# Optimization experiments

Hardware: AMD Instinct MI355X
Metric: run time of the kernel (lower is better)

Reference implementation:

```python
import math
import jax, jax.numpy as jnp
import numpy as np

STEP = 0.1
EPS = 1e-12


def _laplacian(src, dst, n):
    # dense symmetric-normalized Laplacian from COO edge list (symmetrized, 0/1 weights)
    A = jnp.zeros((n, n), dtype=jnp.float32).at[src, dst].set(1.0)
    A = jnp.maximum(A, A.T)
    deg = A.sum(axis=1)
    dinv = jnp.where(deg > 0, 1.0 / jnp.sqrt(jnp.maximum(deg, 1e-12)), 0.0)
    return jnp.eye(n, dtype=jnp.float32) - dinv[:, None] * A * dinv[None, :]


def _filter_bank(L, bs):
    # rational band-pass bank centered at b in arange(0,2.1,STEP):
    # D_b = sqrt(2)*a * inv((L - b I)^4 + a I),  a = (STEP/2)^4
    n = L.shape[0]
    a = (STEP / 2.0) ** 4
    I = jnp.eye(n, dtype=L.dtype)

    def one(b):
        M1 = L - b * I
        P2 = M1 @ M1
        P4 = P2 @ P2
        return math.sqrt(2.0) * a * jnp.linalg.inv(P4 + a * I)

    return jax.vmap(one)(bs)  # [F, n, n]


def _cdist_mean(e):
    # mean pairwise euclidean distance, safe sqrt on the zero diagonal
    d2 = jnp.sum((e[:, None, :] - e[None, :, :]) ** 2, axis=-1)
    d = jnp.sqrt(jnp.where(d2 > 0, d2, 1.0))
    return jnp.where(d2 > 0, d, 0.0).mean()


def setup_inputs() -> dict:
    key = jax.random.key(0)
    k1, k2, k3, k4, k5 = jax.random.split(key, 5)
    B, N, F0, R, E = 64, 128, 32, 1118, 512
    return {
        "x": jax.random.normal(k1, (B, N, F0), dtype=jnp.float32),
        "random_signal": jax.random.normal(k2, (B, N, R), dtype=jnp.float32),
        "C": jax.random.normal(k3, (21, 1), dtype=jnp.float32),
        "edge_src": jax.random.randint(k4, (B, E), 0, N),
        "edge_dst": jax.random.randint(k5, (B, E), 0, N),
        "num_classes": 4,
    }


def reference(x, random_signal, C, edge_src, edge_dst, num_classes):
    B, N, _ = x.shape
    R = random_signal.shape[-1]
    # torch.normal(0, sqrt(1/R)) random signal concatenated to features
    feats = jnp.concatenate([x, random_signal * math.sqrt(1.0 / R)], axis=-1)  # [B,N,F0+R]
    bs = jnp.arange(0.0, 2.1, STEP, dtype=jnp.float32)  # [21]
    Cn = C / jnp.maximum(jnp.linalg.norm(C, axis=0, keepdims=True), EPS)  # F.normalize(C, dim=0)

    def per_graph(src, dst, xg):
        L = _laplacian(src, dst, N)
        D = _filter_bank(L, bs)                      # [F,N,N]
        L_hat = jnp.einsum('fnm,f->nm', D, Cn[:, 0])  # D.permute(1,2,0) @ C, squeezed
        A_hat = jnp.eye(N, dtype=xg.dtype) - L_hat
        y = A_hat @ xg                                # [N, F0+R]
        z = y / jnp.maximum(jnp.linalg.norm(y, axis=1, keepdims=True), EPS)
        logits = z @ z.T                              # decode_all on normalized x
        sp = -jnp.abs(logits).sum() / (N * N)         # -||logits||_1 / n^2
        return y.mean(axis=0), sp

    emb, sp_terms = jax.vmap(per_graph)(edge_src, edge_dst, feats)  # [B,D], [B]

    # faithful repeated in-loop division: s_{i+1} = (s_i + t_i)/B  =>  sum_i t_i * B^{-(B-i)}
    i = jnp.arange(B, dtype=jnp.float32)
    w = jnp.exp(-(B - i) * jnp.log(float(B)))
    sparsity_fwd = jnp.sum(sp_terms * w)

    # labels y = arange(B) % num_classes; one positive group (class members) and
    # one negative group (non-members) per class
    idx = np.arange(B)
    hl1 = jnp.float32(0.0)
    hl2 = jnp.float32(0.0)
    for c in range(num_classes):
        pos = jnp.asarray(idx[idx % num_classes == c])
        neg = jnp.asarray(idx[idx % num_classes != c])
        beta = 1.0 / num_classes + 1e-13  # one group per class
        hl1 = hl1 + (-_cdist_mean(emb[neg])) / beta
        hl2 = hl2 + _cdist_mean(emb[pos])

    Fk = C.shape[0]
    dims = jnp.sqrt(jnp.float32(Fk))
    c_l1 = jnp.sum(jnp.abs(C), axis=0)
    c_l2 = jnp.maximum(jnp.linalg.norm(C, axis=0), EPS)
    sparsity_c = jnp.mean((dims - c_l1 / c_l2) / (dims - 1.0))

    return sparsity_c + hl2 + hl1 + sparsity_fwd
```

## Files before the change

### kernel.cpp

```cpp
#include <hip/hip_runtime.h>
#include <math.h>

#define NN 128
#define SM 129
#define TS 132
#define RS 132
#define SS 17
#define SD 130
#define EP 132

typedef double d4 __attribute__((ext_vector_type(4)));

__global__ __launch_bounds__(256) void k1_lap(
    const int* __restrict__ src, const int* __restrict__ dst,
    int E, float* __restrict__ Lout) {
  extern __shared__ float sm1[];
  float* A    = sm1;
  float* dinv = sm1 + NN * SM;
  const int g   = blockIdx.x;
  const int tid = threadIdx.x;

  for (int e = tid; e < NN * NN; e += 256) {
    int i = e >> 7, j = e & 127;
    A[i * SM + j] = 0.f;
  }
  __syncthreads();
  const int* s = src + (size_t)g * E;
  const int* d = dst + (size_t)g * E;
  for (int e = tid; e < E; e += 256) {
    int a = s[e], b = d[e];
    A[a * SM + b] = 1.f;
    A[b * SM + a] = 1.f;
  }
  __syncthreads();
  if (tid < NN) {
    float acc = 0.f;
    for (int j = 0; j < NN; ++j) acc += A[tid * SM + j];
    dinv[tid] = (acc > 0.f) ? (float)(1.0 / sqrt((double)acc)) : 0.f;
  }
  __syncthreads();
  float* Lg = Lout + (size_t)g * NN * NN;
  for (int e = tid; e < NN * NN; e += 256) {
    int i = e >> 7, j = e & 127;
    Lg[e] = ((i == j) ? 1.f : 0.f) - dinv[i] * dinv[j] * A[i * SM + j];
  }
}

__global__ __launch_bounds__(512, 1) void kpow2(
    const float* __restrict__ L, double* __restrict__ L2) {
  extern __shared__ double Bs[];
  const int bid = blockIdx.x;
  const int g = bid >> 2, q = bid & 3;
  const int tid = threadIdx.x;
  const int wv = tid >> 6, ln = tid & 63;
  const int m  = ln & 15, kq = ln >> 4;
  const int rb = 32 * q + 16 * (wv & 1);
  const int cb0 = 2 * (wv >> 1);

  int rIdx[4], cIdx[4];
  {
    d4 z = {0.0, 0.0, 0.0, 0.0};
    d4 pr = __builtin_amdgcn_mfma_f64_16x16x4f64((double)m, 1.0, z, 0, 0, 0);
    d4 pc = __builtin_amdgcn_mfma_f64_16x16x4f64(1.0, (double)m, z, 0, 0, 0);
#pragma unroll
    for (int r = 0; r < 4; ++r) {
      rIdx[r] = ((int)(pr[r] * 0.25 + 0.5)) & 15;
      cIdx[r] = ((int)(pc[r] * 0.25 + 0.5)) & 15;
    }
  }

  const float* Lg = L + (size_t)g * NN * NN;
  for (int e = tid; e < NN * NN; e += 512) {
    int i = e >> 7, j = e & 127;
    Bs[i * SD + j] = (double)Lg[e];
  }
  __syncthreads();

  d4 acc[2];
#pragma unroll
  for (int c = 0; c < 2; ++c) {
    acc[c][0] = 0.0; acc[c][1] = 0.0; acc[c][2] = 0.0; acc[c][3] = 0.0;
  }
  for (int kc = 0; kc < 32; ++kc) {
    double a = Bs[(rb + m) * SD + 4 * kc + kq];
#pragma unroll
    for (int c = 0; c < 2; ++c) {
      double b = Bs[(4 * kc + kq) * SD + 16 * (cb0 + c) + m];
      acc[c] = __builtin_amdgcn_mfma_f64_16x16x4f64(a, b, acc[c], 0, 0, 0);
    }
  }
  double* out = L2 + (size_t)g * NN * NN;
#pragma unroll
  for (int c = 0; c < 2; ++c)
#pragma unroll
    for (int r = 0; r < 4; ++r)
      out[(rb + rIdx[r]) * NN + 16 * (cb0 + c) + cIdx[r]] = acc[c][r];
}

__global__ __launch_bounds__(512, 1) void kpow34(
    const float* __restrict__ L, const double* __restrict__ L2,
    double* __restrict__ L3, double* __restrict__ L4) {
  extern __shared__ double Bs[];
  const int bid = blockIdx.x;
  const int g = bid >> 2, h = (bid >> 1) & 1, job = bid & 1;
  const int tid = threadIdx.x;
  const int wv = tid >> 6, ln = tid & 63;
  const int m  = ln & 15, kq = ln >> 4;
  const int rb = 64 * h + 16 * (wv & 3);
  const int cb0 = 4 * (wv >> 2);

  int rIdx[4], cIdx[4];
  {
    d4 z = {0.0, 0.0, 0.0, 0.0};
    d4 pr = __builtin_amdgcn_mfma_f64_16x16x4f64((double)m, 1.0, z, 0, 0, 0);
    d4 pc = __builtin_amdgcn_mfma_f64_16x16x4f64(1.0, (double)m, z, 0, 0, 0);
#pragma unroll
    for (int r = 0; r < 4; ++r) {
      rIdx[r] = ((int)(pr[r] * 0.25 + 0.5)) & 15;
      cIdx[r] = ((int)(pc[r] * 0.25 + 0.5)) & 15;
    }
  }

  const float*  Lg  = L  + (size_t)g * NN * NN;
  const double* L2g = L2 + (size_t)g * NN * NN;
  if (job == 0) {
    for (int e = tid; e < NN * NN; e += 512) {
      int i = e >> 7, j = e & 127;
      Bs[i * SD + j] = (double)Lg[e];
    }
  } else {
    for (int e = tid; e < NN * NN; e += 512) {
      int i = e >> 7, j = e & 127;
      Bs[i * SD + j] = L2g[e];
    }
  }
  __syncthreads();

  d4 acc[4];
#pragma unroll
  for (int c = 0; c < 4; ++c) {
    acc[c][0] = 0.0; acc[c][1] = 0.0; acc[c][2] = 0.0; acc[c][3] = 0.0;
  }
  for (int kc = 0; kc < 32; ++kc) {
    double a = L2g[(rb + m) * NN + 4 * kc + kq];
#pragma unroll
    for (int c = 0; c < 4; ++c) {
      double b = Bs[(4 * kc + kq) * SD + 16 * (cb0 + c) + m];
      acc[c] = __builtin_amdgcn_mfma_f64_16x16x4f64(a, b, acc[c], 0, 0, 0);
    }
  }
  double* out = (job == 0 ? L3 : L4) + (size_t)g * NN * NN;
#pragma unroll
  for (int c = 0; c < 4; ++c)
#pragma unroll
    for (int r = 0; r < 4; ++r)
      out[(rb + rIdx[r]) * NN + 16 * (cb0 + c) + cIdx[r]] = acc[c][r];
}

__global__ __launch_bounds__(512, 4) void k2_filter(
    const float* __restrict__ L, const double* __restrict__ L2,
    const double* __restrict__ L3, const double* __restrict__ L4,
    const float* __restrict__ C, int NF, float* __restrict__ W) {
  extern __shared__ char smraw[];
  double* Rp  = (double*)smraw;
  double* Scd = (double*)(smraw + 16 * RS * 8);
  double* Pv  = (double*)(smraw + 16 * RS * 8 + 8 * 16 * SS * 8);

  const int bid = blockIdx.x;
  const int g = bid / NF, f = bid % NF;
  const int tid = threadIdx.x;
  const int wv = tid >> 6, ln = tid & 63;
  const int m  = ln & 15, kq = ln >> 4;
  double* S = Scd + wv * 16 * SS;

  double csum = 0.0;
  for (int q = 0; q < NF; ++q) { double c = (double)C[q]; csum += c * c; }
  double cn = sqrt(csum); if (cn < 1e-12) cn = 1e-12;
  const double a4 = 6.25e-6;
  const double coef = 1.4142135623730951 * a4 * ((double)C[f] / cn);
  const float  bf = (float)((double)f * 0.1);
  const double bb = (double)bf;
  const double c3 = -4.0 * bb;
  const double c2 = 6.0 * bb * bb;
  const double c1 = -4.0 * bb * bb * bb;
  const double c0 = bb * bb * bb * bb + a4;

  int rIdx[4], cIdx[4];
  {
    d4 z = {0.0, 0.0, 0.0, 0.0};
    d4 pr = __builtin_amdgcn_mfma_f64_16x16x4f64((double)m, 1.0, z, 0, 0, 0);
    d4 pc = __builtin_amdgcn_mfma_f64_16x16x4f64(1.0, (double)m, z, 0, 0, 0);
#pragma unroll
    for (int r = 0; r < 4; ++r) {
      rIdx[r] = ((int)(pr[r] * 0.25 + 0.5)) & 15;
      cIdx[r] = ((int)(pc[r] * 0.25 + 0.5)) & 15;
    }
  }

  const float*  Lg  = L  + (size_t)g * NN * NN;
  const double* L2g = L2 + (size_t)g * NN * NN;
  const double* L3g = L3 + (size_t)g * NN * NN;
  const double* L4g = L4 + (size_t)g * NN * NN;
  d4 T[8];
#pragma unroll
  for (int cb = 0; cb < 8; ++cb)
#pragma unroll
    for (int r = 0; r < 4; ++r) {
      int i = 16 * wv + rIdx[r], j = 16 * cb + cIdx[r];
      int idx = i * NN + j;
      double v = L4g[idx];
      v = fma(c3, L3g[idx], v);
      v = fma(c2, L2g[idx], v);
      v = fma(c1, (double)Lg[idx], v);
      if (i == j) v += c0;
      T[cb][r] = v;
    }

#pragma unroll 1
  for (int t = 0; t < 8; ++t) {
    if (wv == t) {
#pragma unroll
      for (int cb = 0; cb < 8; ++cb)
#pragma unroll
        for (int r = 0; r < 4; ++r)
          Rp[rIdx[r] * RS + 16 * cb + cIdx[r]] = T[cb][r];
    }
    __syncthreads();

    if (wv == t) {
      double sr[4];
#pragma unroll
      for (int r = 0; r < 4; ++r) sr[r] = Rp[(4 * r + kq) * RS + 16 * t + m];
#pragma unroll
      for (int k = 0; k < 16; ++k) {
        const int kr = k >> 2, kl = k & 3;
        double pv   = __shfl(sr[kr], 16 * kl + k);
        double rowv = __shfl(sr[kr], 16 * kl + m);
        double cv[4];
#pragma unroll
        for (int r = 0; r < 4; ++r) cv[r] = __shfl(sr[r], 16 * kq + k);
        double dp = 1.0 / pv;
#pragma unroll
        for (int r = 0; r < 4; ++r) {
          int i = 4 * r + kq;
          double nv;
          if (i == k)      nv = (m == k) ? dp : rowv * dp;
          else if (m == k) nv = -cv[r] * dp;
          else             nv = fma(-(cv[r] * dp), rowv, sr[r]);
          sr[r] = nv;
        }
      }
#pragma unroll
      for (int r = 0; r < 4; ++r) Pv[(4 * r + kq) * SS + m] = sr[r];
    }
    __syncthreads();

#pragma unroll
    for (int cb = 0; cb < 8; ++cb) {
      if (cb != t) continue;
      if (wv == t) {
#pragma unroll
        for (int r = 0; r < 4; ++r) T[cb][r] = Pv[rIdx[r] * SS + cIdx[r]];
      } else {
#pragma unroll
        for (int r = 0; r < 4; ++r) S[rIdx[r] * SS + cIdx[r]] = T[cb][r];
        __builtin_amdgcn_wave_barrier();
        d4 ncv = {0.0, 0.0, 0.0, 0.0};
#pragma unroll
        for (int kc = 0; kc < 4; ++kc) {
          double a = S[m * SS + 4 * kc + kq];
          double b = -Pv[(4 * kc + kq) * SS + m];
          ncv = __builtin_amdgcn_mfma_f64_16x16x4f64(a, b, ncv, 0, 0, 0);
        }
        T[cb] = ncv;
        __builtin_amdgcn_wave_barrier();
#pragma unroll
        for (int r = 0; r < 4; ++r) S[rIdx[r] * SS + cIdx[r]] = T[cb][r];
      }
    }
    __builtin_amdgcn_wave_barrier();

    const double* asrc = (wv == t) ? Pv : S;
#pragma unroll
    for (int cb = 0; cb < 8; ++cb) {
      if (cb == t) continue;
      d4 acc;
      if (wv == t) { acc[0] = 0.0; acc[1] = 0.0; acc[2] = 0.0; acc[3] = 0.0; }
      else         { acc = T[cb]; }
#pragma unroll
      for (int kc = 0; kc < 4; ++kc) {
        double a = asrc[m * SS + 4 * kc + kq];
        double b = Rp[(4 * kc + kq) * RS + 16 * cb + m];
        acc = __builtin_amdgcn_mfma_f64_16x16x4f64(a, b, acc, 0, 0, 0);
      }
      T[cb] = acc;
    }
    __syncthreads();
  }

  float* Wg = W + (size_t)g * NN * NN;
#pragma unroll
  for (int cb = 0; cb < 8; ++cb)
#pragma unroll
    for (int r = 0; r < 4; ++r)
      atomicAdd(&Wg[(16 * wv + rIdx[r]) * NN + 16 * cb + cIdx[r]],
                (float)(coef * T[cb][r]));
}

__global__ __launch_bounds__(512, 4) void k3_fused(
    const float* __restrict__ x, const float* __restrict__ rs,
    const float* __restrict__ W, float* __restrict__ G,
    float* __restrict__ emb, int F0, int R, int DTOT, int NCH,
    float rscale) {
  extern __shared__ float sm3[];
  float* ldsX = sm3;
  float* embA = sm3 + NN * TS;
  const int bid = blockIdx.x;
  const int g = bid / NCH;
  const int c = bid % NCH;
  const int d0 = c * 128;
  const int tid = threadIdx.x, tr = tid >> 4, tc = tid & 15;

  const float* xg = x + (size_t)g * NN * F0;
  const float* rg = rs + (size_t)g * NN * R;
  for (int e = tid; e < NN * NN; e += 512) {
    int k = e >> 7, dl = e & 127;
    int d = d0 + dl;
    float v = 0.f;
    if (d < DTOT) v = (d < F0) ? xg[k * F0 + d] : rg[k * R + (d - F0)] * rscale;
    ldsX[k * TS + dl] = v;
  }
  if (tid < NN) embA[tid] = 0.f;
  __syncthreads();

  const float* Wg = W + (size_t)g * NN * NN;
  float acc[4][8];
#pragma unroll
  for (int v = 0; v < 4; ++v)
#pragma unroll
    for (int u = 0; u < 8; ++u) acc[v][u] = 0.f;
  float4 w4 = *(const float4*)(Wg + 4 * tr);
  for (int k = 0; k < NN; ++k) {
    float4 w4n;
    if (k < NN - 1) w4n = *(const float4*)(Wg + (k + 1) * NN + 4 * tr);
    float xv[8];
#pragma unroll
    for (int u = 0; u < 8; ++u) xv[u] = ldsX[k * TS + tc + 16 * u];
    float wvv[4] = {w4.x, w4.y, w4.z, w4.w};
#pragma unroll
    for (int v = 0; v < 4; ++v)
#pragma unroll
      for (int u = 0; u < 8; ++u) acc[v][u] = fmaf(wvv[v], xv[u], acc[v][u]);
    w4 = w4n;
  }
#pragma unroll
  for (int v = 0; v < 4; ++v)
#pragma unroll
    for (int u = 0; u < 8; ++u)
      acc[v][u] = ldsX[(4 * tr + v) * TS + tc + 16 * u] - acc[v][u];

#pragma unroll
  for (int u = 0; u < 8; ++u) {
    float s = acc[0][u] + acc[1][u] + acc[2][u] + acc[3][u];
    atomicAdd(&embA[tc + 16 * u], s);
  }
  __syncthreads();

#pragma unroll
  for (int v = 0; v < 4; ++v)
#pragma unroll
    for (int u = 0; u < 8; ++u)
      ldsX[(tc + 16 * u) * TS + 4 * tr + v] = acc[v][u];
  __syncthreads();

  if (tid < 128) {
    int d = d0 + tid;
    if (d < DTOT) emb[(size_t)g * 1152 + d] = embA[tid] * (1.f / 128.f);
  }

  float gg[4][8];
#pragma unroll
  for (int v = 0; v < 4; ++v)
#pragma unroll
    for (int u = 0; u < 8; ++u) gg[v][u] = 0.f;
  for (int dl = 0; dl < NN; ++dl) {
    float4 a4v = *(const float4*)(ldsX + dl * TS + 4 * tr);
    float bv[8];
#pragma unroll
    for (int u = 0; u < 8; ++u) bv[u] = ldsX[dl * TS + tc + 16 * u];
    float av[4] = {a4v.x, a4v.y, a4v.z, a4v.w};
#pragma unroll
    for (int v = 0; v < 4; ++v)
#pragma unroll
      for (int u = 0; u < 8; ++u) gg[v][u] = fmaf(av[v], bv[u], gg[v][u]);
  }
  float* Gg = G + (size_t)g * NN * NN;
#pragma unroll
  for (int v = 0; v < 4; ++v)
#pragma unroll
    for (int u = 0; u < 8; ++u)
      atomicAdd(&Gg[(4 * tr + v) * NN + tc + 16 * u], gg[v][u]);
}

__global__ __launch_bounds__(256) void k45_fused(
    const float* __restrict__ G, double* __restrict__ spt,
    const float* __restrict__ emb, float* __restrict__ Dm, int DTOT) {
  __shared__ float inr[NN];
  __shared__ double red[4];
  const int bid = blockIdx.x, tid = threadIdx.x;
  if (bid < 64) {
    const int g = bid;
    const float* Gg = G + (size_t)g * NN * NN;
    if (tid < NN) {
      float n = sqrtf(fmaxf(Gg[tid * NN + tid], 0.f));
      inr[tid] = 1.f / fmaxf(n, 1e-12f);
    }
    __syncthreads();
    double s = 0.0;
    for (int e = tid; e < NN * NN; e += 256) {
      int i = e >> 7, j = e & 127;
      s += (double)(fabsf(Gg[e]) * inr[i] * inr[j]);
    }
    for (int off = 32; off; off >>= 1) s += __shfl_down(s, off);
    int wave = tid >> 6, lane = tid & 63;
    if (lane == 0) red[wave] = s;
    __syncthreads();
    if (tid == 0) spt[g] = -(red[0] + red[1] + red[2] + red[3]) / (double)(NN * NN);
  } else {
    const int i = bid - 64;
    const int wv = tid >> 6, l = tid & 63;
    float ei[18];
#pragma unroll
    for (int s = 0; s < 18; ++s) {
      int d = l + 64 * s;
      ei[s] = (d < DTOT) ? emb[(size_t)i * 1152 + d] : 0.f;
    }
    for (int jj = 0; jj < 16; ++jj) {
      int j = 4 * jj + wv;
      float acc = 0.f;
#pragma unroll
      for (int s = 0; s < 18; ++s) {
        int d = l + 64 * s;
        if (d < DTOT) {
          float df = ei[s] - emb[(size_t)j * 1152 + d];
          acc = fmaf(df, df, acc);
        }
      }
      for (int off = 32; off; off >>= 1) acc += __shfl_down(acc, off);
      if (l == 0) Dm[i * 64 + j] = (acc > 0.f) ? sqrtf(acc) : 0.f;
    }
  }
}

__global__ __launch_bounds__(64) void k5b_final(
    const float* __restrict__ Dm, const double* __restrict__ spt,
    const float* __restrict__ C, int NF,
    const int* __restrict__ ncls, float* __restrict__ out) {
  const int lane = threadIdx.x;
  const int nc = ncls[0];
  double spf = spt[lane] * exp(-((double)(64 - lane)) * log(64.0));
  for (int off = 32; off; off >>= 1) spf += __shfl_down(spf, off);

  double hl1 = 0.0, hl2 = 0.0;
  const double beta = 1.0 / (double)nc + 1e-13;
  for (int cc = 0; cc < nc; ++cc) {
    bool ip = (lane % nc) == cc;
    double ps = 0.0, ns = 0.0;
    for (int j = 0; j < 64; ++j) {
      double dv = (double)Dm[lane * 64 + j];
      bool jp = (j % nc) == cc;
      if (ip && jp) ps += dv;
      if (!ip && !jp) ns += dv;
    }
    for (int off = 32; off; off >>= 1) {
      ps += __shfl_down(ps, off);
      ns += __shfl_down(ns, off);
    }
    int npos = 0;
    for (int q = 0; q < 64; ++q) if (q % nc == cc) npos++;
    int nneg = 64 - npos;
    hl2 += ps / ((double)npos * (double)npos);
    hl1 += -(ns / ((double)nneg * (double)nneg)) / beta;
  }
  if (lane == 0) {
    double l1 = 0.0, l2 = 0.0;
    for (int q = 0; q < NF; ++q) { double cv = (double)C[q]; l1 += fabs(cv); l2 += cv * cv; }
    l2 = sqrt(l2); if (l2 < 1e-12) l2 = 1e-12;
    double dims = sqrt((double)NF);
    double sc = (dims - l1 / l2) / (dims - 1.0);
    out[0] = (float)(sc + hl2 + hl1 + spf);
  }
}

extern "C" void kernel_launch(void* const* d_in, const int* in_sizes, int n_in,
                              void* d_out, int out_size, void* d_ws, size_t ws_size,
                              hipStream_t stream) {
  (void)n_in; (void)out_size; (void)ws_size;
  const float* x    = (const float*)d_in[0];
  const float* rs   = (const float*)d_in[1];
  const float* C    = (const float*)d_in[2];
  const int*   esrc = (const int*)d_in[3];
  const int*   edst = (const int*)d_in[4];
  const int*   ncls = (const int*)d_in[5];
  float* out = (float*)d_out;

  const int F0   = in_sizes[0] / (64 * 128);
  const int R    = in_sizes[1] / (64 * 128);
  const int NF   = in_sizes[2];
  const int E    = in_sizes[3] / 64;
  const int DTOT = F0 + R;
  const int NCH  = (DTOT + 127) / 128;
  const float rscale = (float)(1.0 / sqrt((double)R));

  char* ws = (char*)d_ws;
  size_t off = 0;
  float*  L    = (float*)(ws + off);  off += (size_t)64 * NN * NN * 4;
  float*  W    = (float*)(ws + off);  off += (size_t)64 * NN * NN * 4;
  float*  G    = (float*)(ws + off);  off += (size_t)64 * NN * NN * 4;
  double* L2d  = (double*)(ws + off); off += (size_t)64 * NN * NN * 8;
  double* L3d  = (double*)(ws + off); off += (size_t)64 * NN * NN * 8;
  double* L4d  = (double*)(ws + off); off += (size_t)64 * NN * NN * 8;
  float*  emb  = (float*)(ws + off);  off += (size_t)64 * 1152 * 4;
  double* spt  = (double*)(ws + off); off += (size_t)64 * 8;
  float*  Dm   = (float*)(ws + off);  off += (size_t)64 * 64 * 4;

  hipMemsetAsync(W, 0, (size_t)2 * 64 * NN * NN * 4, stream);

  const int lds1 = (NN * SM + NN) * 4;
  const int ldsp = NN * SD * 8;
  const int lds2 = 16 * RS * 8 + 8 * 16 * SS * 8 + 16 * SS * 8;
  const int lds3 = (NN * TS + NN) * 4;
  hipFuncSetAttribute((const void*)k1_lap,    hipFuncAttributeMaxDynamicSharedMemorySize, lds1);
  hipFuncSetAttribute((const void*)kpow2,     hipFuncAttributeMaxDynamicSharedMemorySize, ldsp);
  hipFuncSetAttribute((const void*)kpow34,    hipFuncAttributeMaxDynamicSharedMemorySize, ldsp);
  hipFuncSetAttribute((const void*)k2_filter, hipFuncAttributeMaxDynamicSharedMemorySize, lds2);
  hipFuncSetAttribute((const void*)k3_fused,  hipFuncAttributeMaxDynamicSharedMemorySize, lds3);

  k1_lap<<<64, 256, lds1, stream>>>(esrc, edst, E, L);
  kpow2<<<256, 512, ldsp, stream>>>(L, L2d);
  kpow34<<<256, 512, ldsp, stream>>>(L, L2d, L3d, L4d);
  k2_filter<<<64 * NF, 512, lds2, stream>>>(L, L2d, L3d, L4d, C, NF, W);
  k3_fused<<<64 * NCH, 512, lds3, stream>>>(x, rs, W, G, emb, F0, R, DTOT, NCH, rscale);
  k45_fused<<<128, 256, 0, stream>>>(G, spt, emb, Dm, DTOT);
  k5b_final<<<1, 64, 0, stream>>>(Dm, spt, C, NF, ncls, out);
}
```

Measured before the change: 601.8 us.

## Stage L as float in LDS and split matrix-power kernels into more blocks

The L², L³ and L⁴ kernels now keep L in LDS as fp32 instead of fp64, which halves the shared-memory footprint. Each block also computes fewer output tiles, so twice as many blocks launch with launch bounds that allow 4 blocks per CU. The L4 job now reads both operands of L2 straight from global memory and does not stage them in LDS, trading LDS traffic for cached global loads. The goal is better occupancy and latency hiding in these small fp64 MFMA GEMMs, but per-block staging overhead grows because each block reloads the whole matrix.

New measurement: 606.9 us. Within noise of the previous version (+0.9%).

```diff
diff --git a/kernel.cpp b/kernel.cpp
--- a/kernel.cpp
+++ b/kernel.cpp
@@ -6,7 +6,7 @@
 #define TS 132
 #define RS 132
 #define SS 17
-#define SD 130
+#define SF 132
 #define EP 132
 
 typedef double d4 __attribute__((ext_vector_type(4)));
@@ -46,11 +46,54 @@
   }
 }
 
-__global__ __launch_bounds__(512, 1) void kpow2(
+__global__ __launch_bounds__(512, 4) void kpow2(
     const float* __restrict__ L, double* __restrict__ L2) {
-  extern __shared__ double Bs[];
+  extern __shared__ float Bs[];
   const int bid = blockIdx.x;
-  const int g = bid >> 2, q = bid & 3;
+  const int g = bid >> 3, q = bid & 7;
+  const int tid = threadIdx.x;
+  const int wv = tid >> 6, ln = tid & 63;
+  const int m  = ln & 15, kq = ln >> 4;
+  const int rb = 16 * q;
+  const int cb = wv;
+
+  int rIdx[4], cIdx[4];
+  {
+    d4 z = {0.0, 0.0, 0.0, 0.0};
+    d4 pr = __builtin_amdgcn_mfma_f64_16x16x4f64((double)m, 1.0, z, 0, 0, 0);
+    d4 pc = __builtin_amdgcn_mfma_f64_16x16x4f64(1.0, (double)m, z, 0, 0, 0);
+#pragma unroll
+    for (int r = 0; r < 4; ++r) {
+      rIdx[r] = ((int)(pr[r] * 0.25 + 0.5)) & 15;
+      cIdx[r] = ((int)(pc[r] * 0.25 + 0.5)) & 15;
+    }
+  }
+
+  const float* Lg = L + (size_t)g * NN * NN;
+  for (int e4 = tid; e4 < (NN * NN) / 4; e4 += 512) {
+    int i = e4 >> 5, j4 = (e4 & 31) * 4;
+    *(float4*)(Bs + i * SF + j4) = *(const float4*)(Lg + i * NN + j4);
+  }
+  __syncthreads();
+
+  d4 acc = {0.0, 0.0, 0.0, 0.0};
+  for (int kc = 0; kc < 32; ++kc) {
+    double a = (double)Bs[(rb + m) * SF + 4 * kc + kq];
+    double b = (double)Bs[(4 * kc + kq) * SF + 16 * cb + m];
+    acc = __builtin_amdgcn_mfma_f64_16x16x4f64(a, b, acc, 0, 0, 0);
+  }
+  double* out = L2 + (size_t)g * NN * NN;
+#pragma unroll
+  for (int r = 0; r < 4; ++r)
+    out[(rb + rIdx[r]) * NN + 16 * cb + cIdx[r]] = acc[r];
+}
+
+__global__ __launch_bounds__(512, 4) void kpow34(
+    const float* __restrict__ L, const double* __restrict__ L2,
+    double* __restrict__ L3, double* __restrict__ L4) {
+  extern __shared__ float Bs[];
+  const int bid = blockIdx.x;
+  const int g = bid >> 3, q = (bid >> 1) & 3, job = bid & 1;
   const int tid = threadIdx.x;
   const int wv = tid >> 6, ln = tid & 63;
   const int m  = ln & 15, kq = ln >> 4;
@@ -69,89 +112,43 @@
     }
   }
 
-  const float* Lg = L + (size_t)g * NN * NN;
-  for (int e = tid; e < NN * NN; e += 512) {
-    int i = e >> 7, j = e & 127;
-    Bs[i * SD + j] = (double)Lg[e];
-  }
-  __syncthreads();
-
-  d4 acc[2];
-#pragma unroll
-  for (int c = 0; c < 2; ++c) {
-    acc[c][0] = 0.0; acc[c][1] = 0.0; acc[c][2] = 0.0; acc[c][3] = 0.0;
-  }
-  for (int kc = 0; kc < 32; ++kc) {
-    double a = Bs[(rb + m) * SD + 4 * kc + kq];
-#pragma unroll
-    for (int c = 0; c < 2; ++c) {
-      double b = Bs[(4 * kc + kq) * SD + 16 * (cb0 + c) + m];
-      acc[c] = __builtin_amdgcn_mfma_f64_16x16x4f64(a, b, acc[c], 0, 0, 0);
-    }
-  }
-  double* out = L2 + (size_t)g * NN * NN;
-#pragma unroll
-  for (int c = 0; c < 2; ++c)
-#pragma unroll
-    for (int r = 0; r < 4; ++r)
-      out[(rb + rIdx[r]) * NN + 16 * (cb0 + c) + cIdx[r]] = acc[c][r];
-}
-
-__global__ __launch_bounds__(512, 1) void kpow34(
-    const float* __restrict__ L, const double* __restrict__ L2,
-    double* __restrict__ L3, double* __restrict__ L4) {
-  extern __shared__ double Bs[];
-  const int bid = blockIdx.x;
-  const int g = bid >> 2, h = (bid >> 1) & 1, job = bid & 1;
-  const int tid = threadIdx.x;
-  const int wv = tid >> 6, ln = tid & 63;
-  const int m  = ln & 15, kq = ln >> 4;
-  const int rb = 64 * h + 16 * (wv & 3);
-  const int cb0 = 4 * (wv >> 2);
-
-  int rIdx[4], cIdx[4];
-  {
-    d4 z = {0.0, 0.0, 0.0, 0.0};
-    d4 pr = __builtin_amdgcn_mfma_f64_16x16x4f64((double)m, 1.0, z, 0, 0, 0);
-    d4 pc = __builtin_amdgcn_mfma_f64_16x16x4f64(1.0, (double)m, z, 0, 0, 0);
-#pragma unroll
-    for (int r = 0; r < 4; ++r) {
-      rIdx[r] = ((int)(pr[r] * 0.25 + 0.5)) & 15;
-      cIdx[r] = ((int)(pc[r] * 0.25 + 0.5)) & 15;
-    }
-  }
-
   const float*  Lg  = L  + (size_t)g * NN * NN;
   const double* L2g = L2 + (size_t)g * NN * NN;
   if (job == 0) {
-    for (int e = tid; e < NN * NN; e += 512) {
-      int i = e >> 7, j = e & 127;
-      Bs[i * SD + j] = (double)Lg[e];
+    for (int e4 = tid; e4 < (NN * NN) / 4; e4 += 512) {
+      int i = e4 >> 5, j4 = (e4 & 31) * 4;
+      *(float4*)(Bs + i * SF + j4) = *(const float4*)(Lg + i * NN + j4);
+    }
+  }
+  __syncthreads();
+
+  d4 acc[2];
+#pragma unroll
+  for (int c = 0; c < 2; ++c) {
+    acc[c][0] = 0.0; acc[c][1] = 0.0; acc[c][2] = 0.0; acc[c][3] = 0.0;
+  }
+  if (job == 0) {
+    for (int kc = 0; kc < 32; ++kc) {
+      double a = L2g[(rb + m) * NN + 4 * kc + kq];
+#pragma unroll
+      for (int c = 0; c < 2; ++c) {
+        double b = (double)Bs[(4 * kc + kq) * SF + 16 * (cb0 + c) + m];
+        acc[c] = __builtin_amdgcn_mfma_f64_16x16x4f64(a, b, acc[c], 0, 0, 0);
+      }
     }
   } else {
-    for (int e = tid; e < NN * NN; e += 512) {
-      int i = e >> 7, j = e & 127;
-      Bs[i * SD + j] = L2g[e];
-    }
-  }
-  __syncthreads();
-
-  d4 acc[4];
-#pragma unroll
-  for (int c = 0; c < 4; ++c) {
-    acc[c][0] = 0.0; acc[c][1] = 0.0; acc[c][2] = 0.0; acc[c][3] = 0.0;
-  }
-  for (int kc = 0; kc < 32; ++kc) {
-    double a = L2g[(rb + m) * NN + 4 * kc + kq];
-#pragma unroll
-    for (int c = 0; c < 4; ++c) {
-      double b = Bs[(4 * kc + kq) * SD + 16 * (cb0 + c) + m];
-      acc[c] = __builtin_amdgcn_mfma_f64_16x16x4f64(a, b, acc[c], 0, 0, 0);
+    for (int kc = 0; kc < 32; ++kc) {
+      double a = L2g[(rb + m) * NN + 4 * kc + kq];
+#pragma unroll
+      for (int c = 0; c < 2; ++c) {
+        double b = L2g[(4 * kc + kq) * NN + 16 * (cb0 + c) + m];
+        acc[c] = __builtin_amdgcn_mfma_f64_16x16x4f64(a, b, acc[c], 0, 0, 0);
+      }
     }
   }
   double* out = (job == 0 ? L3 : L4) + (size_t)g * NN * NN;
 #pragma unroll
-  for (int c = 0; c < 4; ++c)
+  for (int c = 0; c < 2; ++c)
 #pragma unroll
     for (int r = 0; r < 4; ++r)
       out[(rb + rIdx[r]) * NN + 16 * (cb0 + c) + cIdx[r]] = acc[c][r];
@@ -527,18 +524,18 @@
   hipMemsetAsync(W, 0, (size_t)2 * 64 * NN * NN * 4, stream);
 
   const int lds1 = (NN * SM + NN) * 4;
-  const int ldsp = NN * SD * 8;
+  const int ldsf = NN * SF * 4;
   const int lds2 = 16 * RS * 8 + 8 * 16 * SS * 8 + 16 * SS * 8;
   const int lds3 = (NN * TS + NN) * 4;
   hipFuncSetAttribute((const void*)k1_lap,    hipFuncAttributeMaxDynamicSharedMemorySize, lds1);
-  hipFuncSetAttribute((const void*)kpow2,     hipFuncAttributeMaxDynamicSharedMemorySize, ldsp);
-  hipFuncSetAttribute((const void*)kpow34,    hipFuncAttributeMaxDynamicSharedMemorySize, ldsp);
+  hipFuncSetAttribute((const void*)kpow2,     hipFuncAttributeMaxDynamicSharedMemorySize, ldsf);
+  hipFuncSetAttribute((const void*)kpow34,    hipFuncAttributeMaxDynamicSharedMemorySize, ldsf);
   hipFuncSetAttribute((const void*)k2_filter, hipFuncAttributeMaxDynamicSharedMemorySize, lds2);
   hipFuncSetAttribute((const void*)k3_fused,  hipFuncAttributeMaxDynamicSharedMemorySize, lds3);
 
   k1_lap<<<64, 256, lds1, stream>>>(esrc, edst, E, L);
-  kpow2<<<256, 512, ldsp, stream>>>(L, L2d);
-  kpow34<<<256, 512, ldsp, stream>>>(L, L2d, L3d, L4d);
+  kpow2<<<512, 512, ldsf, stream>>>(L, L2d);
+  kpow34<<<512, 512, ldsf, stream>>>(L, L2d, L3d, L4d);
   k2_filter<<<64 * NF, 512, lds2, stream>>>(L, L2d, L3d, L4d, C, NF, W);
   k3_fused<<<64 * NCH, 512, lds3, stream>>>(x, rs, W, G, emb, F0, R, DTOT, NCH, rscale);
   k45_fused<<<128, 256, 0, stream>>>(G, spt, emb, Dm, DTOT);
```
